# Optimization experiments

Measured on AMD Instinct MI355X. Metric: run time of the kernel, lower is better.

The kernel has to match this reference:

```python
import jax, jax.numpy as jnp
import numpy as np

NUM_HEADS = 8
HEAD_SPLITS = [2, 3, 3]          # heads per window size
WINDOWS = [3, 5, 7]


def _dwconv(x, w, b, k):
    """Depthwise 2D conv, SAME padding. x:[B,C,H,W], w:[C,1,k,k], b:[C]."""
    p = k // 2
    y = jax.lax.conv_general_dilated(
        x, w, window_strides=(1, 1), padding=[(p, p), (p, p)],
        dimension_numbers=("NCHW", "OIHW", "NCHW"),
        feature_group_count=x.shape[1])
    return y + b[None, :, None, None]


def setup_inputs() -> dict:
    key = jax.random.key(0)
    ks = jax.random.split(key, 8)
    B, N, C = 8, 3137, 768
    c = C // NUM_HEADS  # 96
    inp = {
        "x": jax.random.normal(ks[0], (B, N, C), dtype=jnp.float32),
        "qkv_w": jax.random.normal(ks[1], (3 * C, C), dtype=jnp.float32) * 0.02,
        "qkv_b": jnp.zeros((3 * C,), dtype=jnp.float32),
        "proj_w": jax.random.normal(ks[2], (C, C), dtype=jnp.float32) * 0.02,
        "proj_b": jnp.zeros((C,), dtype=jnp.float32),
        "conv3_w": jax.random.normal(ks[3], (2 * c, 1, 3, 3), dtype=jnp.float32) * 0.02,
        "conv3_b": jnp.zeros((2 * c,), dtype=jnp.float32),
        "conv5_w": jax.random.normal(ks[4], (3 * c, 1, 5, 5), dtype=jnp.float32) * 0.02,
        "conv5_b": jnp.zeros((3 * c,), dtype=jnp.float32),
        "conv7_w": jax.random.normal(ks[5], (3 * c, 1, 7, 7), dtype=jnp.float32) * 0.02,
        "conv7_b": jnp.zeros((3 * c,), dtype=jnp.float32),
        "H": 56,
        "W": 56,
    }
    return inp


def reference(x, qkv_w, qkv_b, proj_w, proj_b,
              conv3_w, conv3_b, conv5_w, conv5_b, conv7_w, conv7_b, H, W):
    B, N, C = x.shape
    h = NUM_HEADS
    c = C // h
    scale = c ** -0.5

    # qkv projection -> q,k,v each [B,h,N,c]
    qkv = x @ qkv_w.T + qkv_b
    qkv = qkv.reshape(B, N, 3, h, c).transpose(2, 0, 3, 1, 4)
    q, k, v = qkv[0], qkv[1], qkv[2]

    # factorized attention: softmax over token axis of k
    k_softmax = jax.nn.softmax(k, axis=2)
    kv = jnp.einsum("bhnc,bhnd->bhcd", k_softmax, v)       # [B,h,c,c]
    factor_att = jnp.einsum("bhnc,bhcd->bhnd", q, kv)      # [B,h,N,c]

    # ConvRelPosEnc on image tokens
    q_img = q[:, :, 1:, :]                                  # [B,h,HW,c]
    v_img = v[:, :, 1:, :]                                  # [B,h,HW,c]
    v_img = v_img.transpose(0, 1, 3, 2).reshape(B, h * c, H, W)
    splits = np.cumsum([s * c for s in HEAD_SPLITS])[:-1].tolist()
    v2, v5, v7 = jnp.split(v_img, splits, axis=1)
    conv_v = jnp.concatenate([
        _dwconv(v2, conv3_w, conv3_b, 3),
        _dwconv(v5, conv5_w, conv5_b, 5),
        _dwconv(v7, conv7_w, conv7_b, 7),
    ], axis=1)                                              # [B,h*c,H,W]
    conv_v = conv_v.reshape(B, h, c, H * W).transpose(0, 1, 3, 2)  # [B,h,HW,c]
    ev = q_img * conv_v
    crpe = jnp.pad(ev, ((0, 0), (0, 0), (1, 0), (0, 0)))    # zero row for cls token

    out = scale * factor_att + crpe                         # [B,h,N,c]
    out = out.transpose(0, 2, 1, 3).reshape(B, N, C)
    out = out @ proj_w.T + proj_b
    return out
```

## Files before the change

### kernel.cpp

```cpp
#include <hip/hip_runtime.h>
#include <hip/hip_bf16.h>


#define BB 8
#define NN 3137
#define HH 8
#define CH 96
#define HW 3136
#define IMG 56
#define MTOK (BB*NN)
#define NCHK 16
#define CTOK 197

typedef __bf16 bf16x8 __attribute__((ext_vector_type(8)));
typedef unsigned short u16x8 __attribute__((ext_vector_type(8)));
typedef unsigned short u16x4 __attribute__((ext_vector_type(4)));
typedef float  f32x4  __attribute__((ext_vector_type(4)));
typedef float  f32x8  __attribute__((ext_vector_type(8)));

__device__ __forceinline__ void gl_lds16(const void* g, void* l) {
    __builtin_amdgcn_global_load_lds(
        (const __attribute__((address_space(1))) unsigned int*)g,
        (__attribute__((address_space(3))) unsigned int*)l, 16, 0, 0);
}
__device__ __forceinline__ unsigned ldsaddr(const void* p) {
    return (unsigned)(size_t)(const __attribute__((address_space(3))) char*)p;
}
__device__ __forceinline__ bf16x8 ds_rd128(unsigned a) {
    bf16x8 r;
    asm volatile("ds_read_b128 %0, %1" : "=v"(r) : "v"(a));
    return r;
}

__global__ __launch_bounds__(256) void cvt_bf16(
    const float* __restrict__ in, unsigned short* __restrict__ out, int n8)
{
    const int i = blockIdx.x * 256 + threadIdx.x;
    if (i < n8) {
        const f32x8 v = ((const f32x8*)in)[i];
        ((u16x8*)out)[i] = (u16x8)__builtin_convertvector(v, bf16x8);
    }
}

__global__ __launch_bounds__(512, 2) void gemm256(
    const unsigned short* __restrict__ A,
    const unsigned short* __restrict__ W,
    const float* __restrict__ bias,
    unsigned short* __restrict__ C,
    int lda, int ldw, int ldc, int M, int NT)
{
    __shared__ alignas(16) unsigned short lds[2*2*2*8192];
    const int tid = threadIdx.x;
    const int nwg = gridDim.x * gridDim.y;
    const int orig = blockIdx.y * gridDim.x + blockIdx.x;
    const int q8 = nwg >> 3, r8 = nwg & 7;
    const int xcd = orig & 7, off = orig >> 3;
    const int wgid = (xcd < r8 ? xcd*(q8+1) : r8*(q8+1) + (xcd-r8)*q8) + off;
    const int n0 = (wgid % gridDim.x) * 256;
    const int m0 = (wgid / gridDim.x) * 256;

    const int lane = tid & 63, wave = tid >> 6;
    const int lr = lane & 15, quad = lane >> 4;
    const int wm2 = wave >> 2;
    const int wn4 = wave & 3;
    const int bh  = wn4 >> 1;
    const int brow = (wn4 & 1) * 64;

    const int srow0 = tid >> 3, skc0 = tid & 7;
    const int srow1 = (tid + 512) >> 3, skc1 = tid & 7;
    const int kce0 = (skc0 ^ (srow0 & 7)) * 8;
    const int kce1 = (skc1 ^ (srow1 & 7)) * 8;

    auto stage = [&](int p, int mat, int h, int t) {
        unsigned short* dst = lds + (((p*2 + mat)*2 + h) << 13);
        const int kb = t * 64;
        if (mat == 0) {
            int g0 = m0 + h*128 + srow0; if (g0 > M-1) g0 = M-1;
            int g1 = m0 + h*128 + srow1; if (g1 > M-1) g1 = M-1;
            gl_lds16(A + (size_t)g0*lda + kb + kce0, dst + tid*8);
            gl_lds16(A + (size_t)g1*lda + kb + kce1, dst + (tid+512)*8);
        } else {
            const int g0 = n0 + h*128 + srow0;
            const int g1 = n0 + h*128 + srow1;
            gl_lds16(W + (size_t)g0*ldw + kb + kce0, dst + tid*8);
            gl_lds16(W + (size_t)g1*ldw + kb + kce1, dst + (tid+512)*8);
        }
    };

    const unsigned ldsB = ldsaddr(lds);
    const unsigned swz0 = (unsigned)(((0*4 + quad) ^ (lr & 7)) << 4);
    const unsigned swz1 = (unsigned)(((1*4 + quad) ^ (lr & 7)) << 4);

    stage(0,1,0,0); stage(0,1,1,0);
    stage(0,0,0,0); stage(0,0,1,0);
    stage(1,1,0,1); stage(1,1,1,1);
    asm volatile("s_waitcnt vmcnt(4)" ::: "memory");
    __builtin_amdgcn_s_barrier();

    f32x4 acc[8][4] = {};
    bf16x8 bfr[4][2], af[2][2];
    for (int t = 0; t < NT; ++t) {
        const int p = t & 1;
        const unsigned Ab = ldsB + ((unsigned)((p*2 + 0)*2 + wm2) << 14) + (unsigned)lr*128;
        const unsigned Bb = ldsB + ((unsigned)((p*2 + 1)*2 + bh ) << 14) + (unsigned)(brow + lr)*128;
#pragma unroll
        for (int q = 0; q < 4; ++q) {
            if (q == 0) {
#pragma unroll
                for (int j = 0; j < 4; ++j) {
                    bfr[j][0] = ds_rd128(Bb + j*16*128 + swz0);
                    bfr[j][1] = ds_rd128(Bb + j*16*128 + swz1);
                }
            }
#pragma unroll
            for (int ii = 0; ii < 2; ++ii) {
                const unsigned ra = Ab + (q*32 + ii*16)*128;
                af[ii][0] = ds_rd128(ra + swz0);
                af[ii][1] = ds_rd128(ra + swz1);
            }
            if (q == 0)      { if (t+1 < NT) stage(p^1, 0, 0, t+1); }
            else if (q == 1) { if (t+1 < NT) stage(p^1, 0, 1, t+1); }
            else if (q == 2) { if (t+2 < NT) stage(p, 1, 0, t+2); }
            else             { if (t+2 < NT) stage(p, 1, 1, t+2); }
            __builtin_amdgcn_s_barrier();
            asm volatile("s_waitcnt lgkmcnt(0)" ::: "memory");
            __builtin_amdgcn_sched_barrier(0);
            __builtin_amdgcn_s_setprio(1);
#pragma unroll
            for (int ii = 0; ii < 2; ++ii)
#pragma unroll
                for (int j = 0; j < 4; ++j)
#pragma unroll
                    for (int ks = 0; ks < 2; ++ks)
                        acc[q*2+ii][j] = __builtin_amdgcn_mfma_f32_16x16x32_bf16(
                            bfr[j][ks], af[ii][ks], acc[q*2+ii][j], 0, 0, 0);
            __builtin_amdgcn_s_setprio(0);
            if (q == 3) {
                if (t+2 < NT)      asm volatile("s_waitcnt vmcnt(4)" ::: "memory");
                else if (t+1 < NT) asm volatile("s_waitcnt vmcnt(0)" ::: "memory");
            }
            __builtin_amdgcn_s_barrier();
        }
    }

#pragma unroll
    for (int i = 0; i < 8; ++i) {
        const int row = m0 + wm2*128 + i*16 + lr;
        if (row < M) {
#pragma unroll
            for (int j = 0; j < 4; ++j) {
                const int col = n0 + wn4*64 + j*16 + quad*4;
                const f32x4 bv = *(const f32x4*)(bias + col);
                u16x4 st;
#pragma unroll
                for (int r = 0; r < 4; ++r)
                    st[r] = __hip_bfloat16_raw(__float2bfloat16(acc[i][j][r] + bv[r])).x;
                *(u16x4*)&C[(size_t)row*ldc + col] = st;
            }
        }
    }
}

template<bool OUT_F32>
__global__ __launch_bounds__(256) void gemm_bt(
    const unsigned short* __restrict__ A, int lda,
    const unsigned short* __restrict__ W,
    const float* __restrict__ bias,
    void* __restrict__ Cptr, int ldc,
    int M, int Nd, int K)
{
    __shared__ alignas(16) unsigned short As[128*32];
    __shared__ alignas(16) unsigned short Bs[128*32];
    const int tid  = threadIdx.x;
    const int nwg = gridDim.x * gridDim.y;
    int orig = blockIdx.y * gridDim.x + blockIdx.x;
    const int q8 = nwg >> 3, r8 = nwg & 7;
    const int xcd = orig & 7, off = orig >> 3;
    const int wgid = (xcd < r8 ? xcd*(q8+1) : r8*(q8+1) + (xcd-r8)*q8) + off;
    const int n0   = (wgid % gridDim.x) * 128;
    const int m0   = (wgid / gridDim.x) * 128;
    const int lane = tid & 63;
    const int wave = tid >> 6;
    const int wm   = (wave >> 1) * 64;
    const int wn   = (wave & 1) * 64;
    const int lr   = lane & 15;
    const int quad = lane >> 4;

    const int r0 = tid >> 2, c0 = (tid & 3) * 8;
    const int r1 = r0 + 64;
    int am0 = m0 + r0; if (am0 > M-1) am0 = M-1;
    int am1 = m0 + r1; if (am1 > M-1) am1 = M-1;
    const unsigned short* a0 = A + (size_t)am0*lda + c0;
    const unsigned short* a1 = A + (size_t)am1*lda + c0;
    const unsigned short* w0 = W + (size_t)(n0+r0)*K + c0;
    const unsigned short* w1 = W + (size_t)(n0+r1)*K + c0;
    unsigned short* lA0 = As + tid*8;
    unsigned short* lA1 = As + (tid+256)*8;
    unsigned short* lB0 = Bs + tid*8;
    unsigned short* lB1 = Bs + (tid+256)*8;

    f32x4 acc[4][4] = {};
    for (int k0 = 0; k0 < K; k0 += 32) {
        __syncthreads();
        gl_lds16(a0 + k0, lA0);
        gl_lds16(a1 + k0, lA1);
        gl_lds16(w0 + k0, lB0);
        gl_lds16(w1 + k0, lB1);
        asm volatile("s_waitcnt vmcnt(0)" ::: "memory");
        __syncthreads();
        bf16x8 af[4], bfr[4];
#pragma unroll
        for (int i = 0; i < 4; ++i) {
            af[i]  = *(const bf16x8*)(As + (wm + i*16 + lr)*32 + quad*8);
            bfr[i] = *(const bf16x8*)(Bs + (wn + i*16 + lr)*32 + quad*8);
        }
#pragma unroll
        for (int i = 0; i < 4; ++i)
#pragma unroll
            for (int j = 0; j < 4; ++j)
                acc[i][j] = __builtin_amdgcn_mfma_f32_16x16x32_bf16(bfr[j], af[i], acc[i][j], 0, 0, 0);
    }
#pragma unroll
    for (int i = 0; i < 4; ++i) {
        const int row = m0 + wm + i*16 + lr;
        if (row < M) {
#pragma unroll
            for (int j = 0; j < 4; ++j) {
                const int col = n0 + wn + j*16 + quad*4;
                const f32x4 bv = *(const f32x4*)(bias + col);
                f32x4 v;
#pragma unroll
                for (int r = 0; r < 4; ++r) v[r] = acc[i][j][r] + bv[r];
                if (OUT_F32) {
                    *(f32x4*)&((float*)Cptr)[(size_t)row*ldc + col] = v;
                } else {
                    u16x4 st;
#pragma unroll
                    for (int r = 0; r < 4; ++r)
                        st[r] = __hip_bfloat16_raw(__float2bfloat16(v[r])).x;
                    *(u16x4*)&((__hip_bfloat16*)Cptr)[(size_t)row*ldc + col] = st;
                }
            }
        }
    }
}

__global__ __launch_bounds__(256) void kv_accum(
    const __hip_bfloat16* __restrict__ qkv,
    float* __restrict__ kvp,
    float* __restrict__ spart)
{
    const int bh = blockIdx.x;
    const int chunk = blockIdx.y;
    const int b = bh >> 3, h = bh & 7;
    const int nstart = chunk * CTOK;
    int nend = nstart + CTOK; if (nend > NN) nend = NN;
    __shared__ float krow[16][96], vrow[16][96];
    __shared__ float sacc[192][8];
    const int t = threadIdx.x;

    const int sr = t / 12, sc = (t % 12) * 8;
    const __hip_bfloat16* kb = qkv + (size_t)b*NN*2304 + 768 + h*96;
    const __hip_bfloat16* vb = kb + 768;
    float ssum[8] = {};

    const int ci = (t >> 4) * 6;
    const int di = (t & 15) * 6;
    float acc[6][6] = {};
    for (int n = nstart; n < nend; n += 16) {
        __syncthreads();
        if (t < 192) {
            const int nn = n + sr;
            if (nn < nend) {
                const bf16x8 kr = *(const bf16x8*)(kb + (size_t)nn*2304 + sc);
                const bf16x8 vr = *(const bf16x8*)(vb + (size_t)nn*2304 + sc);
                const f32x8 kf = __builtin_convertvector(kr, f32x8);
                const f32x8 vf = __builtin_convertvector(vr, f32x8);
                f32x8 ke;
#pragma unroll
                for (int j = 0; j < 8; ++j) { ke[j] = __expf(kf[j]); ssum[j] += ke[j]; }
                *(f32x4*)&krow[sr][sc]   = *(const f32x4*)&ke;
                *(f32x4*)&krow[sr][sc+4] = *((const f32x4*)&ke + 1);
                *(f32x4*)&vrow[sr][sc]   = *(const f32x4*)&vf;
                *(f32x4*)&vrow[sr][sc+4] = *((const f32x4*)&vf + 1);
            } else {
                const f32x4 z = {0.f,0.f,0.f,0.f};
                *(f32x4*)&krow[sr][sc] = z; *(f32x4*)&krow[sr][sc+4] = z;
                *(f32x4*)&vrow[sr][sc] = z; *(f32x4*)&vrow[sr][sc+4] = z;
            }
        }
        __syncthreads();
#pragma unroll 4
        for (int r = 0; r < 16; ++r) {
            float kf[6], vf[6];
#pragma unroll
            for (int i = 0; i < 6; ++i) kf[i] = krow[r][ci+i];
#pragma unroll
            for (int j = 0; j < 6; ++j) vf[j] = vrow[r][di+j];
#pragma unroll
            for (int i = 0; i < 6; ++i)
#pragma unroll
                for (int j = 0; j < 6; ++j)
                    acc[i][j] += kf[i] * vf[j];
        }
    }
    float* outp = kvp + (size_t)(chunk*64 + bh)*9216;
#pragma unroll
    for (int i = 0; i < 6; ++i)
#pragma unroll
        for (int j = 0; j < 6; ++j)
            outp[(ci+i)*96 + (di+j)] = acc[i][j];
    if (t < 192) {
#pragma unroll
        for (int j = 0; j < 8; ++j) sacc[t][j] = ssum[j];
    }
    __syncthreads();
    if (t < 96) {
        const int g = t >> 3, e = t & 7;
        float S = 0.f;
#pragma unroll
        for (int m = 0; m < 16; ++m) S += sacc[g + 12*m][e];
        spart[(size_t)(chunk*64 + bh)*96 + t] = S;
    }
}

__global__ __launch_bounds__(256) void kv_prep(
    const float* __restrict__ kvp, const float* __restrict__ spart,
    unsigned short* __restrict__ kvb)
{
    const int bh = blockIdx.x, y = blockIdx.y;
    __shared__ float sinv[24];
    const int t = threadIdx.x;
    const int cbase = y * 24;
    if (t < 24) {
        float S = 0.f;
#pragma unroll
        for (int ch = 0; ch < NCHK; ++ch)
            S += spart[(size_t)(ch*64 + bh)*96 + cbase + t];
        sinv[t] = 1.0f / S;
    }
    __syncthreads();
    unsigned short* dst = kvb + (size_t)bh*19968;
    for (int i = t; i < 2304; i += 256) {
        const int ii = y*2304 + i;
        const int c = ii / 96, d = ii % 96;
        float v = 0.f;
#pragma unroll
        for (int ch = 0; ch < NCHK; ++ch)
            v += kvp[(size_t)(ch*64 + bh)*9216 + ii];
        v *= sinv[c - cbase];
        const __hip_bfloat16 hb = __float2bfloat16(v);
        const float lo = v - __bfloat162float(hb);
        const __hip_bfloat16 lb = __float2bfloat16(lo);
        dst[d*104 + c]        = __hip_bfloat16_raw(hb).x;
        dst[9984 + d*104 + c] = __hip_bfloat16_raw(lb).x;
    }
}

__global__ __launch_bounds__(256) void fatt(
    const __hip_bfloat16* __restrict__ qkv,
    const unsigned short* __restrict__ kvb,
    const __hip_bfloat16* __restrict__ cv,
    __hip_bfloat16* __restrict__ att)
{
    __shared__ alignas(16) unsigned short kvs[2*96*104];
    const int tile = blockIdx.x, h = blockIdx.y, b = blockIdx.z;
    const int t = threadIdx.x, lane = t & 63, wave = t >> 6;
    const int lr = lane & 15, quad = lane >> 4;

    const unsigned short* kg = kvb + (size_t)(b*8 + h)*19968;
#pragma unroll
    for (int s = 0; s < 10; ++s) {
        const int slot = t + s*256;
        if (slot < 2496) gl_lds16(kg + slot*8, kvs + slot*8);
    }

    const int n0 = tile*128 + wave*32;
    const unsigned short* qbu = (const unsigned short*)qkv + (size_t)b*NN*2304 + h*96;
    bf16x8 af[2][3];
#pragma unroll
    for (int i = 0; i < 2; ++i) {
        int n = n0 + i*16 + lr; if (n > NN-1) n = NN-1;
#pragma unroll
        for (int kk = 0; kk < 3; ++kk)
            af[i][kk] = *(const bf16x8*)(qbu + (size_t)n*2304 + kk*32 + quad*8);
    }
    asm volatile("s_waitcnt vmcnt(0)" ::: "memory");
    __syncthreads();

    f32x4 acc[2][6] = {};
#pragma unroll
    for (int j = 0; j < 6; ++j) {
#pragma unroll
        for (int kk = 0; kk < 3; ++kk) {
            const bf16x8 bhh = *(const bf16x8*)(kvs + (j*16 + lr)*104 + kk*32 + quad*8);
            const bf16x8 bll = *(const bf16x8*)(kvs + 9984 + (j*16 + lr)*104 + kk*32 + quad*8);
#pragma unroll
            for (int i = 0; i < 2; ++i) {
                acc[i][j] = __builtin_amdgcn_mfma_f32_16x16x32_bf16(af[i][kk], bhh, acc[i][j], 0, 0, 0);
                acc[i][j] = __builtin_amdgcn_mfma_f32_16x16x32_bf16(af[i][kk], bll, acc[i][j], 0, 0, 0);
            }
        }
    }

    const float scale = 0.10206207261596577f;
    const __hip_bfloat16* qb  = (const __hip_bfloat16*)qbu;
    const __hip_bfloat16* cvb = cv + (size_t)(b*8 + h)*HW*96;
    __hip_bfloat16* ab = att + (size_t)b*NN*2304 + h*96;
#pragma unroll
    for (int i = 0; i < 2; ++i) {
#pragma unroll
        for (int j = 0; j < 6; ++j) {
            const int col = j*16 + lr;
#pragma unroll
            for (int r = 0; r < 4; ++r) {
                const int n = n0 + i*16 + quad*4 + r;
                if (n < NN) {
                    float v = scale * acc[i][j][r];
                    if (n > 0) {
                        const float qv = __bfloat162float(qb[(size_t)n*2304 + col]);
                        v += qv * __bfloat162float(cvb[(size_t)(n-1)*96 + col]);
                    }
                    ab[(size_t)n*2304 + col] = __float2bfloat16(v);
                }
            }
        }
    }
}

template<int KS>
__device__ __forceinline__ void dw_band(
    float (*vt)[64][36],
    const __hip_bfloat16* __restrict__ vbase,
    const float* __restrict__ wp, float bv,
    __hip_bfloat16* __restrict__ cvo,
    int y0)
{
    constexpr int P = KS/2;
    const int t = threadIdx.x;
    float wr[KS*KS];
#pragma unroll
    for (int i = 0; i < KS*KS; ++i) wr[i] = wp[i];

    const int spx = t >> 2, sc0 = (t & 3) * 8;
    const int ch = t & 31, xs = t >> 5;
    const int xbase = xs*7 + 4 - P;

#pragma unroll
    for (int r = -P; r < P; ++r) {
        const int y = y0 + r;
        if (t < 224) {
            f32x8 v8 = {0,0,0,0,0,0,0,0};
            if ((unsigned)y < (unsigned)IMG) {
                const bf16x8 rv = *(const bf16x8*)(vbase + (size_t)(y*IMG + spx)*2304 + sc0);
                v8 = __builtin_convertvector(rv, f32x8);
            }
            float* dst = &vt[(y+8)&7][spx+4][sc0];
            *(f32x4*)dst     = *(f32x4*)&v8;
            *(f32x4*)(dst+4) = *((f32x4*)&v8 + 1);
        }
    }

    for (int yy = y0; yy < y0 + 14; ++yy) {
        {
            const int y = yy + P;
            if (t < 224) {
                f32x8 v8 = {0,0,0,0,0,0,0,0};
                if ((unsigned)y < (unsigned)IMG) {
                    const bf16x8 rv = *(const bf16x8*)(vbase + (size_t)(y*IMG + spx)*2304 + sc0);
                    v8 = __builtin_convertvector(rv, f32x8);
                }
                float* dst = &vt[(y+8)&7][spx+4][sc0];
                *(f32x4*)dst     = *(f32x4*)&v8;
                *(f32x4*)(dst+4) = *((f32x4*)&v8 + 1);
            }
        }
        __syncthreads();
        float acc[7];
#pragma unroll
        for (int j = 0; j < 7; ++j) acc[j] = bv;
        for (int dy = 0; dy < KS; ++dy) {
            const float* rowp = &vt[(yy + dy - P + 8) & 7][0][ch] + xbase*36;
            float win[7 + 2*P];
#pragma unroll
            for (int i = 0; i < 7 + 2*P; ++i) win[i] = rowp[i*36];
#pragma unroll
            for (int dx = 0; dx < KS; ++dx)
#pragma unroll
                for (int j = 0; j < 7; ++j)
                    acc[j] += wr[dy*KS+dx] * win[j+dx];
        }
        const int p0 = yy*IMG + xs*7;
#pragma unroll
        for (int j = 0; j < 7; ++j)
            cvo[(size_t)(p0 + j)*96] = __float2bfloat16(acc[j]);
        __syncthreads();
    }
}

__global__ __launch_bounds__(256) void dwconv2(
    const __hip_bfloat16* __restrict__ qkv,
    const float* __restrict__ w3, const float* __restrict__ b3,
    const float* __restrict__ w5, const float* __restrict__ b5,
    const float* __restrict__ w7, const float* __restrict__ b7,
    __hip_bfloat16* __restrict__ cv)
{
    __shared__ float vt[8][64][36];
    const int band = blockIdx.x, grp = blockIdx.y, b = blockIdx.z;
    const int t = threadIdx.x;
    {
        const int s = t >> 5, i = t & 31;
        const int xi = i >> 2;
        const int xp = (xi < 4) ? xi : 56 + xi;
        const int c0 = (i & 3) * 8;
        const f32x4 z = {0.f, 0.f, 0.f, 0.f};
        *(f32x4*)&vt[s][xp][c0]     = z;
        *(f32x4*)&vt[s][xp][c0+4]   = z;
    }
    const int chbase = grp * 32;
    const int wg = chbase + (t & 31);
    const int h = wg / 96, d = wg % 96;
    const int y0 = band * 14;
    const __hip_bfloat16* vbase = qkv + (size_t)b*NN*2304 + 2304 + 1536 + chbase;
    __hip_bfloat16* cvo = cv + ((size_t)(b*8 + h)*HW)*96 + d;
    if (grp < 6)        dw_band<3>(vt, vbase, w3 + wg*9,        b3[wg],     cvo, y0);
    else if (grp < 15)  dw_band<5>(vt, vbase, w5 + (wg-192)*25, b5[wg-192], cvo, y0);
    else                dw_band<7>(vt, vbase, w7 + (wg-480)*49, b7[wg-480], cvo, y0);
}

extern "C" void kernel_launch(void* const* d_in, const int* in_sizes, int n_in,
                              void* d_out, int out_size, void* d_ws, size_t ws_size,
                              hipStream_t stream)
{
    const float* x      = (const float*)d_in[0];
    const float* qkv_w  = (const float*)d_in[1];
    const float* qkv_b  = (const float*)d_in[2];
    const float* proj_w = (const float*)d_in[3];
    const float* proj_b = (const float*)d_in[4];
    const float* w3 = (const float*)d_in[5];
    const float* b3 = (const float*)d_in[6];
    const float* w5 = (const float*)d_in[7];
    const float* b5 = (const float*)d_in[8];
    const float* w7 = (const float*)d_in[9];
    const float* b7 = (const float*)d_in[10];
    float* out = (float*)d_out;

    char* ws = (char*)d_ws;
    const size_t QKV_B = (size_t)MTOK * 2304 * 2;
    const size_t XB_B  = (size_t)MTOK * 768 * 2;
    const size_t SH_B  = XB_B;
    const size_t KV_B  = (size_t)64 * 9216 * 4;
    const size_t ST_B  = 49152;
    const size_t WB_B  = (size_t)2304 * 768 * 2;
    const size_t PW_B  = (size_t)768 * 768 * 2;
    if (ws_size < QKV_B + SH_B + KV_B + ST_B + WB_B + PW_B) return;
    __hip_bfloat16* qkv  = (__hip_bfloat16*)ws;
    unsigned short* xb   = (unsigned short*)(ws + QKV_B);
    float*          kvp  = (float*)(ws + QKV_B);
    float*          spart= (float*)(ws + QKV_B + (size_t)NCHK*64*9216*4);
    __hip_bfloat16* cv   = (__hip_bfloat16*)(ws + QKV_B);
    unsigned short* wb   = (unsigned short*)(ws + QKV_B + SH_B + KV_B + ST_B);
    unsigned short* pwb  = (unsigned short*)(ws + QKV_B + SH_B + KV_B + ST_B + WB_B);

    cvt_bf16<<<(MTOK*768/8 + 255)/256, 256, 0, stream>>>(x, xb, MTOK*768/8);
    cvt_bf16<<<(2304*768/8 + 255)/256, 256, 0, stream>>>(qkv_w, wb, 2304*768/8);
    cvt_bf16<<<(768*768/8 + 255)/256, 256, 0, stream>>>(proj_w, pwb, 768*768/8);
    gemm256<<<dim3(9, 99), 512, 0, stream>>>(
        xb, wb, qkv_b, (unsigned short*)qkv, 768, 768, 2304, MTOK, 768/64);
    kv_accum<<<dim3(64, NCHK), 256, 0, stream>>>(qkv, kvp, spart);
    kv_prep<<<dim3(64, 4), 256, 0, stream>>>(kvp, spart, wb);
    dwconv2<<<dim3(4, 24, 8), 256, 0, stream>>>(qkv, w3, b3, w5, b5, w7, b7, cv);
    fatt<<<dim3(25, 8, 8), 256, 0, stream>>>(qkv, wb, cv,
                                             (__hip_bfloat16*)ws + 768);
    gemm_bt<true><<<dim3(6, 197), 256, 0, stream>>>(
        (const unsigned short*)ws + 768, 2304, pwb, proj_b, out, 768,
        MTOK, 768, 768);
}
```

Baseline: 502.1 us.

## Use MFMA for K^T V accumulation and stage QKV GEMM epilogue through LDS

Replaces the scalar FP32 outer-product kv_accum kernel with an MFMA bf16 kernel (kv_mfma) that stores exp(k) and v transposed in LDS. Chunking changes to 13 chunks of 256 tokens with 384-thread blocks. The gemm256 epilogue now writes bf16 results into LDS and then does coalesced 16-byte row stores, replacing scattered 8-byte stores. Rounding exp(k) to bf16 before the matmul lowers precision, and the epilogue adds barriers.

```diff
diff --git a/kernel.cpp b/kernel.cpp
--- a/kernel.cpp
+++ b/kernel.cpp
@@ -9,8 +9,8 @@
 #define HW 3136
 #define IMG 56
 #define MTOK (BB*NN)
-#define NCHK 16
-#define CTOK 197
+#define NCHK 13
+#define CTOK 256
 
 typedef __bf16 bf16x8 __attribute__((ext_vector_type(8)));
 typedef unsigned short u16x8 __attribute__((ext_vector_type(8)));
@@ -30,6 +30,9 @@
     bf16x8 r;
     asm volatile("ds_read_b128 %0, %1" : "=v"(r) : "v"(a));
     return r;
+}
+__device__ __forceinline__ unsigned short bf16r(float x) {
+    return __hip_bfloat16_raw(__float2bfloat16(x)).x;
 }
 
 __global__ __launch_bounds__(256) void cvt_bf16(
@@ -144,18 +147,33 @@
     }
 
 #pragma unroll
-    for (int i = 0; i < 8; ++i) {
-        const int row = m0 + wm2*128 + i*16 + lr;
-        if (row < M) {
-#pragma unroll
-            for (int j = 0; j < 4; ++j) {
-                const int col = n0 + wn4*64 + j*16 + quad*4;
-                const f32x4 bv = *(const f32x4*)(bias + col);
-                u16x4 st;
-#pragma unroll
-                for (int r = 0; r < 4; ++r)
-                    st[r] = __hip_bfloat16_raw(__float2bfloat16(acc[i][j][r] + bv[r])).x;
-                *(u16x4*)&C[(size_t)row*ldc + col] = st;
+    for (int hh = 0; hh < 2; ++hh) {
+        __builtin_amdgcn_s_barrier();
+        if (wm2 == hh) {
+#pragma unroll
+            for (int i = 0; i < 8; ++i) {
+                const int row = i*16 + lr;
+#pragma unroll
+                for (int j = 0; j < 4; ++j) {
+                    const int col = wn4*64 + j*16 + quad*4;
+                    const f32x4 bv = *(const f32x4*)(bias + n0 + col);
+                    u16x4 st;
+#pragma unroll
+                    for (int r = 0; r < 4; ++r)
+                        st[r] = bf16r(acc[i][j][r] + bv[r]);
+                    *(u16x4*)&lds[row*264 + col] = st;
+                }
+            }
+        }
+        __builtin_amdgcn_s_barrier();
+#pragma unroll
+        for (int k = 0; k < 8; ++k) {
+            const int lrow = wave*16 + k*2 + (lane >> 5);
+            const int grow = m0 + hh*128 + lrow;
+            const int coff = (lane & 31) * 8;
+            if (grow < M) {
+                const u16x8 vv = *(const u16x8*)&lds[lrow*264 + coff];
+                *(u16x8*)&C[(size_t)grow*ldc + n0 + coff] = vv;
             }
         }
     }
@@ -236,8 +254,7 @@
                 } else {
                     u16x4 st;
 #pragma unroll
-                    for (int r = 0; r < 4; ++r)
-                        st[r] = __hip_bfloat16_raw(__float2bfloat16(v[r])).x;
+                    for (int r = 0; r < 4; ++r) st[r] = bf16r(v[r]);
                     *(u16x4*)&((__hip_bfloat16*)Cptr)[(size_t)row*ldc + col] = st;
                 }
             }
@@ -245,81 +262,68 @@
     }
 }
 
-__global__ __launch_bounds__(256) void kv_accum(
+__global__ __launch_bounds__(384) void kv_mfma(
     const __hip_bfloat16* __restrict__ qkv,
     float* __restrict__ kvp,
     float* __restrict__ spart)
 {
-    const int bh = blockIdx.x;
-    const int chunk = blockIdx.y;
+    __shared__ alignas(16) unsigned short ekT[96*40];
+    __shared__ alignas(16) unsigned short vT [96*40];
+    __shared__ float sacc[384][8];
+    const int bh = blockIdx.x, chunk = blockIdx.y;
     const int b = bh >> 3, h = bh & 7;
     const int nstart = chunk * CTOK;
-    int nend = nstart + CTOK; if (nend > NN) nend = NN;
-    __shared__ float krow[16][96], vrow[16][96];
-    __shared__ float sacc[192][8];
     const int t = threadIdx.x;
-
-    const int sr = t / 12, sc = (t % 12) * 8;
-    const __hip_bfloat16* kb = qkv + (size_t)b*NN*2304 + 768 + h*96;
+    const int lane = t & 63, wave = t >> 6;
+    const int lr = lane & 15, quad = lane >> 4;
+    const int sr = t / 12, g = t % 12;
+    const __hip_bfloat16* kb = qkv + (size_t)b*NN*2304 + 768 + h*96 + g*8;
     const __hip_bfloat16* vb = kb + 768;
-    float ssum[8] = {};
-
-    const int ci = (t >> 4) * 6;
-    const int di = (t & 15) * 6;
-    float acc[6][6] = {};
-    for (int n = nstart; n < nend; n += 16) {
+
+    float ssum[8] = {0.f,0.f,0.f,0.f,0.f,0.f,0.f,0.f};
+    f32x4 acc[6] = {};
+#pragma unroll 1
+    for (int s = 0; s < 8; ++s) {
+        const int n = nstart + s*32 + sr;
         __syncthreads();
-        if (t < 192) {
-            const int nn = n + sr;
-            if (nn < nend) {
-                const bf16x8 kr = *(const bf16x8*)(kb + (size_t)nn*2304 + sc);
-                const bf16x8 vr = *(const bf16x8*)(vb + (size_t)nn*2304 + sc);
+        {
+            f32x8 ke = {0,0,0,0,0,0,0,0};
+            u16x8 vraw = {0,0,0,0,0,0,0,0};
+            if (n < NN) {
+                const bf16x8 kr = *(const bf16x8*)(kb + (size_t)n*2304);
+                vraw = *(const u16x8*)(vb + (size_t)n*2304);
                 const f32x8 kf = __builtin_convertvector(kr, f32x8);
-                const f32x8 vf = __builtin_convertvector(vr, f32x8);
-                f32x8 ke;
 #pragma unroll
                 for (int j = 0; j < 8; ++j) { ke[j] = __expf(kf[j]); ssum[j] += ke[j]; }
-                *(f32x4*)&krow[sr][sc]   = *(const f32x4*)&ke;
-                *(f32x4*)&krow[sr][sc+4] = *((const f32x4*)&ke + 1);
-                *(f32x4*)&vrow[sr][sc]   = *(const f32x4*)&vf;
-                *(f32x4*)&vrow[sr][sc+4] = *((const f32x4*)&vf + 1);
-            } else {
-                const f32x4 z = {0.f,0.f,0.f,0.f};
-                *(f32x4*)&krow[sr][sc] = z; *(f32x4*)&krow[sr][sc+4] = z;
-                *(f32x4*)&vrow[sr][sc] = z; *(f32x4*)&vrow[sr][sc+4] = z;
+            }
+#pragma unroll
+            for (int e = 0; e < 8; ++e) {
+                ekT[(g*8+e)*40 + sr] = bf16r(ke[e]);
+                vT [(g*8+e)*40 + sr] = vraw[e];
             }
         }
         __syncthreads();
-#pragma unroll 4
-        for (int r = 0; r < 16; ++r) {
-            float kf[6], vf[6];
-#pragma unroll
-            for (int i = 0; i < 6; ++i) kf[i] = krow[r][ci+i];
-#pragma unroll
-            for (int j = 0; j < 6; ++j) vf[j] = vrow[r][di+j];
-#pragma unroll
-            for (int i = 0; i < 6; ++i)
-#pragma unroll
-                for (int j = 0; j < 6; ++j)
-                    acc[i][j] += kf[i] * vf[j];
+        const bf16x8 afr = *(const bf16x8*)(ekT + (wave*16 + lr)*40 + quad*8);
+#pragma unroll
+        for (int fj = 0; fj < 6; ++fj) {
+            const bf16x8 bfrg = *(const bf16x8*)(vT + (fj*16 + lr)*40 + quad*8);
+            acc[fj] = __builtin_amdgcn_mfma_f32_16x16x32_bf16(afr, bfrg, acc[fj], 0, 0, 0);
         }
     }
     float* outp = kvp + (size_t)(chunk*64 + bh)*9216;
 #pragma unroll
-    for (int i = 0; i < 6; ++i)
-#pragma unroll
-        for (int j = 0; j < 6; ++j)
-            outp[(ci+i)*96 + (di+j)] = acc[i][j];
-    if (t < 192) {
-#pragma unroll
-        for (int j = 0; j < 8; ++j) sacc[t][j] = ssum[j];
-    }
+    for (int fj = 0; fj < 6; ++fj)
+#pragma unroll
+        for (int r = 0; r < 4; ++r)
+            outp[(wave*16 + quad*4 + r)*96 + fj*16 + lr] = acc[fj][r];
+#pragma unroll
+    for (int j = 0; j < 8; ++j) sacc[t][j] = ssum[j];
     __syncthreads();
     if (t < 96) {
-        const int g = t >> 3, e = t & 7;
+        const int g2 = t >> 3, e2 = t & 7;
         float S = 0.f;
 #pragma unroll
-        for (int m = 0; m < 16; ++m) S += sacc[g + 12*m][e];
+        for (int rr = 0; rr < 32; ++rr) S += sacc[rr*12 + g2][e2];
         spart[(size_t)(chunk*64 + bh)*96 + t] = S;
     }
 }
@@ -351,9 +355,8 @@
         v *= sinv[c - cbase];
         const __hip_bfloat16 hb = __float2bfloat16(v);
         const float lo = v - __bfloat162float(hb);
-        const __hip_bfloat16 lb = __float2bfloat16(lo);
         dst[d*104 + c]        = __hip_bfloat16_raw(hb).x;
-        dst[9984 + d*104 + c] = __hip_bfloat16_raw(lb).x;
+        dst[9984 + d*104 + c] = bf16r(lo);
     }
 }
 
@@ -567,7 +570,7 @@
     cvt_bf16<<<(768*768/8 + 255)/256, 256, 0, stream>>>(proj_w, pwb, 768*768/8);
     gemm256<<<dim3(9, 99), 512, 0, stream>>>(
         xb, wb, qkv_b, (unsigned short*)qkv, 768, 768, 2304, MTOK, 768/64);
-    kv_accum<<<dim3(64, NCHK), 256, 0, stream>>>(qkv, kvp, spart);
+    kv_mfma<<<dim3(64, NCHK), 384, 0, stream>>>(qkv, kvp, spart);
     kv_prep<<<dim3(64, 4), 256, 0, stream>>>(kvp, spart, wb);
     dwconv2<<<dim3(4, 24, 8), 256, 0, stream>>>(qkv, w3, b3, w5, b5, w7, b7, cv);
     fatt<<<dim3(25, 8, 8), 256, 0, stream>>>(qkv, wb, cv,
```

Measured after the change: 467.7 us. 1.07x faster.
